# Kernel optimization log

Hardware: AMD Instinct MI355X
Metric: run time of the kernel (lower is better)

Reference implementation:

```python
import jax, jax.numpy as jnp
import numpy as np


def setup_inputs() -> dict:
    key = jax.random.key(0)
    kA, kB = jax.random.split(key)
    A = jax.random.normal(kA, (8, 256, 256, 64), dtype=jnp.float32)
    B = jax.random.normal(kB, (8, 256, 256, 64), dtype=jnp.float32)
    return {"A": A, "B": B}


def reference(A, B):
    # t-product: FFT along tube dim, batched complex matmul per frequency, IFFT.
    Af = jnp.fft.fft(A, axis=-1)          # [b, n1, n2, n3] complex
    Bf = jnp.fft.fft(B, axis=-1)          # [b, n2, n,  n3] complex
    # single batched complex GEMM over (b, n3) instead of a python loop
    Cf = jnp.einsum('bijk,bjnk->bink', Af, Bf)  # [b, n1, n, n3]
    C = jnp.fft.ifft(Cf, axis=-1)
    return jnp.real(C)
```

## Files before the change

### kernel.cpp

```cpp
#include <hip/hip_runtime.h>
#include <hip/hip_bf16.h>
#include <stdint.h>


typedef __bf16 bf16x8 __attribute__((ext_vector_type(8)));
typedef float f32x4 __attribute__((ext_vector_type(4)));

constexpr float TWC[32] = {
  1.0f, 0.99518472667f, 0.98078528040f, 0.95694033573f,
  0.92387953251f, 0.88192126435f, 0.83146961230f, 0.77301045336f,
  0.70710678119f, 0.63439328416f, 0.55557023302f, 0.47139673683f,
  0.38268343236f, 0.29028467725f, 0.19509032202f, 0.09801714033f,
  0.0f, -0.09801714033f, -0.19509032202f, -0.29028467725f,
  -0.38268343236f, -0.47139673683f, -0.55557023302f, -0.63439328416f,
  -0.70710678119f, -0.77301045336f, -0.83146961230f, -0.88192126435f,
  -0.92387953251f, -0.95694033573f, -0.98078528040f, -0.99518472667f
};
constexpr float TWS[32] = {
  0.0f, 0.09801714033f, 0.19509032202f, 0.29028467725f,
  0.38268343236f, 0.47139673683f, 0.55557023302f, 0.63439328416f,
  0.70710678119f, 0.77301045336f, 0.83146961230f, 0.88192126435f,
  0.92387953251f, 0.95694033573f, 0.98078528040f, 0.99518472667f,
  1.0f, 0.99518472667f, 0.98078528040f, 0.95694033573f,
  0.92387953251f, 0.88192126435f, 0.83146961230f, 0.77301045336f,
  0.70710678119f, 0.63439328416f, 0.55557023302f, 0.47139673683f,
  0.38268343236f, 0.29028467725f, 0.19509032202f, 0.09801714033f
};

__device__ __forceinline__ constexpr int rev6(int x) {
  int r = 0;
  for (int b = 0; b < 6; ++b) r = (r << 1) | ((x >> b) & 1);
  return r;
}

template <int SIGN>
__device__ __forceinline__ void fft64(float* re, float* im) {
#pragma unroll
  for (int i = 0; i < 64; ++i) {
    const int j = rev6(i);
    if (j > i) {
      float tr = re[i]; re[i] = re[j]; re[j] = tr;
      float ti = im[i]; im[i] = im[j]; im[j] = ti;
    }
  }
#pragma unroll
  for (int s = 0; s < 6; ++s) {
    const int half = 1 << s;
    const int m = 2 << s;
    const int tstep = 64 >> (s + 1);
#pragma unroll
    for (int kb = 0; kb < 64; kb += m) {
#pragma unroll
      for (int t = 0; t < half; ++t) {
        const int idx = t * tstep;
        const float wr = TWC[idx];
        const float wi = SIGN * TWS[idx];
        const int a = kb + t, b = a + half;
        const float xr = re[b] * wr - im[b] * wi;
        const float xi = re[b] * wi + im[b] * wr;
        re[b] = re[a] - xr; im[b] = im[a] - xi;
        re[a] += xr;        im[a] += xi;
      }
    }
  }
}

__global__ __launch_bounds__(64) void fft_a_kernel(const float* __restrict__ A,
                                                   __bf16* __restrict__ Af) {
  const int blk = blockIdx.x;
  const int jblk = blk & 3;
  const int bi = blk >> 2;
  const int l = threadIdx.x;
  const int lm16 = l & 15, lq4 = l >> 4;
  __shared__ float lds[64 * 68];
  const float* src = A + (((size_t)bi * 256) + (size_t)jblk * 64) * 64;
#pragma unroll
  for (int it = 0; it < 16; ++it) {
    const int r = it * 4 + lq4;
    const float4 v = *(const float4*)&src[(size_t)r * 64 + lm16 * 4];
    *(float4*)&lds[r * 68 + lm16 * 4] = v;
  }
  __syncthreads();
  float re[64], im[64];
#pragma unroll
  for (int e = 0; e < 64; ++e) { re[e] = lds[l * 68 + e]; im[e] = 0.0f; }
  fft64<-1>(re, im);
  const int b = bi >> 8, i = bi & 255;
  const int j = jblk * 64 + l;
#pragma unroll
  for (int k = 0; k <= 32; ++k) {
    const size_t plane = (size_t)(b * 33 + k) * (256 * 512);
    Af[plane + (size_t)i * 512 + j]       = (__bf16)re[k];
    Af[plane + (size_t)i * 512 + 256 + j] = (__bf16)im[k];
  }
}

__global__ __launch_bounds__(64) void fft_b_kernel(const float* __restrict__ B,
                                                   __bf16* __restrict__ Bn) {
  const int blk = blockIdx.x;
  const int jblk = blk & 3;
  const int bn = blk >> 2;
  const int b = bn >> 8, n = bn & 255;
  const int l = threadIdx.x;
  const int lm16 = l & 15, lq4 = l >> 4;
  __shared__ float lds[64 * 68];
#pragma unroll
  for (int it = 0; it < 16; ++it) {
    const int r = it * 4 + lq4;
    const size_t base = (((size_t)b * 256 + (size_t)(jblk * 64 + r)) * 256 + n) * 64;
    const float4 v = *(const float4*)&B[base + lm16 * 4];
    *(float4*)&lds[r * 68 + lm16 * 4] = v;
  }
  __syncthreads();
  float re[64], im[64];
#pragma unroll
  for (int e = 0; e < 64; ++e) { re[e] = lds[l * 68 + e]; im[e] = 0.0f; }
  fft64<-1>(re, im);
  const int j = jblk * 64 + l;
#pragma unroll
  for (int k = 0; k <= 32; ++k) {
    const size_t plane = (size_t)(b * 33 + k) * (256 * 512);
    Bn[plane + (size_t)n * 512 + j]       = (__bf16)re[k];
    Bn[plane + (size_t)n * 512 + 256 + j] = (__bf16)im[k];
  }
}

__device__ __forceinline__ void gload_lds16(const void* g, void* l) {
  __builtin_amdgcn_global_load_lds(
      (const __attribute__((address_space(1))) void*)g,
      (__attribute__((address_space(3))) void*)l, 16, 0, 0);
}

__device__ __forceinline__ bf16x8 neg8(bf16x8 v) {
  union { bf16x8 b; uint32_t u[4]; } x;
  x.b = v;
  x.u[0] ^= 0x80008000u; x.u[1] ^= 0x80008000u;
  x.u[2] ^= 0x80008000u; x.u[3] ^= 0x80008000u;
  return x.b;
}

__global__ __launch_bounds__(256, 2) void gemm_kernel(const __bf16* __restrict__ Af,
                                                      const __bf16* __restrict__ Bn,
                                                      __bf16* __restrict__ Cf) {
  const int bid = blockIdx.x;
  const int x = bid & 7, qx = bid >> 3;
  const int g = x * 33 + (qx >> 2);
  const int tile = qx & 3;
  const int i0 = (tile >> 1) * 128, n0 = (tile & 1) * 128;

  const int tid = threadIdx.x;
  const int lane = tid & 63, wv = tid >> 6;
  const int wm = wv >> 1, wn = wv & 1;
  const int lm = lane & 15, qq = lane >> 4;

  __shared__ __bf16 S[4][128 * 32];

  const __bf16* aPlane = Af + (size_t)g * (256 * 512);
  const __bf16* bPlane = Bn + (size_t)g * (256 * 512);

  const int row_in = lane >> 2;
  const int c_phys = lane & 3;
  const int c_log = c_phys ^ ((row_in >> 1) & 3);
  const __bf16* stageBase = (wv < 2 ? aPlane : bPlane);
  const int r0 = (wv < 2 ? i0 : n0);
  const int colOff = (wv & 1) * 256;
  const __bf16* gsrc0 = stageBase + (size_t)(r0 + row_in) * 512 + colOff + c_log * 8;
  char* ldst = (char*)&S[wv][0];

  f32x4 acc_r[4][4], acc_i[4][4];
#pragma unroll
  for (int mi = 0; mi < 4; ++mi)
#pragma unroll
    for (int ni = 0; ni < 4; ++ni) {
      acc_r[mi][ni] = f32x4{0.f, 0.f, 0.f, 0.f};
      acc_i[mi][ni] = f32x4{0.f, 0.f, 0.f, 0.f};
    }

  int aoff[4], boff[4];
#pragma unroll
  for (int mi = 0; mi < 4; ++mi) {
    const int R = wm * 64 + mi * 16 + lm;
    aoff[mi] = R * 32 + ((qq ^ ((R >> 1) & 3)) * 8);
  }
#pragma unroll
  for (int ni = 0; ni < 4; ++ni) {
    const int R = wn * 64 + ni * 16 + lm;
    boff[ni] = R * 32 + ((qq ^ ((R >> 1) & 3)) * 8);
  }

  for (int kt = 0; kt < 8; ++kt) {
#pragma unroll
    for (int p = 0; p < 8; ++p) {
      gload_lds16(gsrc0 + (size_t)p * 16 * 512 + kt * 32, ldst + p * 1024);
    }
    __syncthreads();

    bf16x8 ar[4], ai[4], br[4], bi[4], nbi[4];
#pragma unroll
    for (int mi = 0; mi < 4; ++mi) {
      ar[mi] = *(const bf16x8*)&S[0][aoff[mi]];
      ai[mi] = *(const bf16x8*)&S[1][aoff[mi]];
    }
#pragma unroll
    for (int ni = 0; ni < 4; ++ni) {
      br[ni]  = *(const bf16x8*)&S[2][boff[ni]];
      bi[ni]  = *(const bf16x8*)&S[3][boff[ni]];
      nbi[ni] = neg8(bi[ni]);
    }
#pragma unroll
    for (int mi = 0; mi < 4; ++mi)
#pragma unroll
      for (int ni = 0; ni < 4; ++ni) {
        acc_r[mi][ni] = __builtin_amdgcn_mfma_f32_16x16x32_bf16(ar[mi], br[ni],  acc_r[mi][ni], 0, 0, 0);
        acc_r[mi][ni] = __builtin_amdgcn_mfma_f32_16x16x32_bf16(ai[mi], nbi[ni], acc_r[mi][ni], 0, 0, 0);
        acc_i[mi][ni] = __builtin_amdgcn_mfma_f32_16x16x32_bf16(ar[mi], bi[ni],  acc_i[mi][ni], 0, 0, 0);
        acc_i[mi][ni] = __builtin_amdgcn_mfma_f32_16x16x32_bf16(ai[mi], br[ni],  acc_i[mi][ni], 0, 0, 0);
      }
    __syncthreads();
  }

  __bf16* cPlane = Cf + (size_t)g * (256 * 512);
#pragma unroll
  for (int mi = 0; mi < 4; ++mi)
#pragma unroll
    for (int ni = 0; ni < 4; ++ni) {
      const int col = n0 + wn * 64 + ni * 16 + lm;
#pragma unroll
      for (int r = 0; r < 4; ++r) {
        const int row = i0 + wm * 64 + mi * 16 + qq * 4 + r;
        cPlane[(size_t)row * 512 + col]       = (__bf16)acc_r[mi][ni][r];
        cPlane[(size_t)row * 512 + 256 + col] = (__bf16)acc_i[mi][ni][r];
      }
    }
}

__global__ __launch_bounds__(64) void ifft_kernel(const __bf16* __restrict__ Cf,
                                                  float* __restrict__ C) {
  const int blk = blockIdx.x;
  const int nblk = blk & 3;
  const int bi = blk >> 2;
  const int b = bi >> 8, i = bi & 255;
  const int l = threadIdx.x;
  const int lm16 = l & 15, lq4 = l >> 4;
  const int n = nblk * 64 + l;
  float re[64], im[64];
#pragma unroll
  for (int k = 0; k <= 32; ++k) {
    const size_t plane = (size_t)(b * 33 + k) * (256 * 512);
    const float cr = (float)Cf[plane + (size_t)i * 512 + n];
    const float ci = (float)Cf[plane + (size_t)i * 512 + 256 + n];
    re[k] = cr; im[k] = ci;
    if (k >= 1 && k <= 31) { re[64 - k] = cr; im[64 - k] = -ci; }
  }
  fft64<1>(re, im);
  __shared__ float lds[64 * 68];
#pragma unroll
  for (int t = 0; t < 64; ++t) lds[l * 68 + t] = re[t] * (1.0f / 64.0f);
  __syncthreads();
  const size_t base = (((size_t)b * 256 + i) * 256 + (size_t)nblk * 64) * 64;
#pragma unroll
  for (int it = 0; it < 16; ++it) {
    const int r = it * 4 + lq4;
    const float4 v = *(const float4*)&lds[r * 68 + lm16 * 4];
    *(float4*)&C[base + (size_t)r * 64 + lm16 * 4] = v;
  }
}

extern "C" void kernel_launch(void* const* d_in, const int* in_sizes, int n_in,
                              void* d_out, int out_size, void* d_ws, size_t ws_size,
                              hipStream_t stream) {
  const float* A = (const float*)d_in[0];
  const float* B = (const float*)d_in[1];
  float* C = (float*)d_out;

  char* ws = (char*)d_ws;
  const size_t planeBytes = (size_t)264 * 256 * 512 * 2;
  __bf16* Af = (__bf16*)ws;
  __bf16* Bn = (__bf16*)(ws + planeBytes);
  __bf16* Cf = (__bf16*)(ws + 2 * planeBytes);

  fft_a_kernel<<<8192, 64, 0, stream>>>(A, Af);
  fft_b_kernel<<<8192, 64, 0, stream>>>(B, Bn);
  gemm_kernel<<<1056, 256, 0, stream>>>(Af, Bn, Cf);
  ifft_kernel<<<8192, 64, 0, stream>>>(Cf, C);
}
```

Baseline: 419.1 us.

## Merge forward FFT kernels and vectorize bf16 spectral stores/loads via LDS staging

Merges the A and B forward FFT kernels into a single launch. Each kernel now stages its bf16 spectra through LDS so it writes 16-byte coalesced chunks instead of scattered 2-byte stores. The inverse FFT kernel now loads its bf16 input with global_load_lds 16-byte transfers into LDS instead of per-element 2-byte global loads. The aim is to cut memory transaction overhead and one launch, at the cost of extra LDS round trips and barriers.

```diff
diff --git a/kernel.cpp b/kernel.cpp
--- a/kernel.cpp
+++ b/kernel.cpp
@@ -65,70 +65,81 @@
   }
 }
 
-__global__ __launch_bounds__(64) void fft_a_kernel(const float* __restrict__ A,
-                                                   __bf16* __restrict__ Af) {
-  const int blk = blockIdx.x;
-  const int jblk = blk & 3;
-  const int bi = blk >> 2;
-  const int l = threadIdx.x;
-  const int lm16 = l & 15, lq4 = l >> 4;
-  __shared__ float lds[64 * 68];
-  const float* src = A + (((size_t)bi * 256) + (size_t)jblk * 64) * 64;
-#pragma unroll
-  for (int it = 0; it < 16; ++it) {
-    const int r = it * 4 + lq4;
-    const float4 v = *(const float4*)&src[(size_t)r * 64 + lm16 * 4];
-    *(float4*)&lds[r * 68 + lm16 * 4] = v;
-  }
-  __syncthreads();
-  float re[64], im[64];
-#pragma unroll
-  for (int e = 0; e < 64; ++e) { re[e] = lds[l * 68 + e]; im[e] = 0.0f; }
-  fft64<-1>(re, im);
-  const int b = bi >> 8, i = bi & 255;
-  const int j = jblk * 64 + l;
-#pragma unroll
-  for (int k = 0; k <= 32; ++k) {
-    const size_t plane = (size_t)(b * 33 + k) * (256 * 512);
-    Af[plane + (size_t)i * 512 + j]       = (__bf16)re[k];
-    Af[plane + (size_t)i * 512 + 256 + j] = (__bf16)im[k];
-  }
-}
-
-__global__ __launch_bounds__(64) void fft_b_kernel(const float* __restrict__ B,
-                                                   __bf16* __restrict__ Bn) {
-  const int blk = blockIdx.x;
-  const int jblk = blk & 3;
-  const int bn = blk >> 2;
-  const int b = bn >> 8, n = bn & 255;
-  const int l = threadIdx.x;
-  const int lm16 = l & 15, lq4 = l >> 4;
-  __shared__ float lds[64 * 68];
-#pragma unroll
-  for (int it = 0; it < 16; ++it) {
-    const int r = it * 4 + lq4;
-    const size_t base = (((size_t)b * 256 + (size_t)(jblk * 64 + r)) * 256 + n) * 64;
-    const float4 v = *(const float4*)&B[base + lm16 * 4];
-    *(float4*)&lds[r * 68 + lm16 * 4] = v;
-  }
-  __syncthreads();
-  float re[64], im[64];
-#pragma unroll
-  for (int e = 0; e < 64; ++e) { re[e] = lds[l * 68 + e]; im[e] = 0.0f; }
-  fft64<-1>(re, im);
-  const int j = jblk * 64 + l;
-#pragma unroll
-  for (int k = 0; k <= 32; ++k) {
-    const size_t plane = (size_t)(b * 33 + k) * (256 * 512);
-    Bn[plane + (size_t)n * 512 + j]       = (__bf16)re[k];
-    Bn[plane + (size_t)n * 512 + 256 + j] = (__bf16)im[k];
-  }
-}
-
 __device__ __forceinline__ void gload_lds16(const void* g, void* l) {
   __builtin_amdgcn_global_load_lds(
       (const __attribute__((address_space(1))) void*)g,
       (__attribute__((address_space(3))) void*)l, 16, 0, 0);
+}
+
+__global__ __launch_bounds__(64) void fft_ab_kernel(const float* __restrict__ A,
+                                                    const float* __restrict__ B,
+                                                    __bf16* __restrict__ Af,
+                                                    __bf16* __restrict__ Bn) {
+  const int blk0 = blockIdx.x;
+  const bool isA = blk0 < 8192;
+  const int blk = blk0 & 8191;
+  const int jblk = blk & 3;
+  const int bi = blk >> 2;
+  const int b = bi >> 8, rc = bi & 255;
+  const int l = threadIdx.x;
+  const int lm16 = l & 15, lq4 = l >> 4;
+
+  __shared__ float lds[64 * 68];
+
+  const float* srcBase = isA
+      ? (A + ((size_t)bi * 256 + (size_t)jblk * 64) * 64)
+      : (B + (((size_t)b * 256 + (size_t)jblk * 64) * 256 + rc) * 64);
+  const size_t strideR = isA ? 64 : (size_t)256 * 64;
+  __bf16* dst = isA ? Af : Bn;
+
+#pragma unroll
+  for (int it = 0; it < 16; ++it) {
+    const int r = it * 4 + lq4;
+    const float4 v = *(const float4*)&srcBase[(size_t)r * strideR + lm16 * 4];
+    *(float4*)&lds[r * 68 + lm16 * 4] = v;
+  }
+  __syncthreads();
+  float re[64], im[64];
+#pragma unroll
+  for (int e = 0; e < 64; ++e) { re[e] = lds[l * 68 + e]; im[e] = 0.0f; }
+  __syncthreads();
+  fft64<-1>(re, im);
+
+  uint32_t* out32 = (uint32_t*)lds;
+#pragma unroll
+  for (int k = 0; k <= 32; ++k) {
+    union { __bf16 h[2]; uint32_t u; } pk;
+    pk.h[0] = (__bf16)re[k]; pk.h[1] = (__bf16)im[k];
+    out32[k * 68 + l] = pk.u;
+  }
+  __syncthreads();
+
+  const int hiIm = (l >> 3) & 1;
+  const int j0c = (l & 7) * 8;
+#pragma unroll
+  for (int it = 0; it < 9; ++it) {
+    const int k = it * 4 + lq4;
+    if (it < 8 || l < 16) {
+      const uint4 q0 = *(const uint4*)&out32[k * 68 + j0c];
+      const uint4 q1 = *(const uint4*)&out32[k * 68 + j0c + 4];
+      uint32_t d0, d1, d2, d3;
+      if (!hiIm) {
+        d0 = (q0.x & 0xffffu) | (q0.y << 16);
+        d1 = (q0.z & 0xffffu) | (q0.w << 16);
+        d2 = (q1.x & 0xffffu) | (q1.y << 16);
+        d3 = (q1.z & 0xffffu) | (q1.w << 16);
+      } else {
+        d0 = (q0.x >> 16) | (q0.y & 0xffff0000u);
+        d1 = (q0.z >> 16) | (q0.w & 0xffff0000u);
+        d2 = (q1.x >> 16) | (q1.y & 0xffff0000u);
+        d3 = (q1.z >> 16) | (q1.w & 0xffff0000u);
+      }
+      const size_t elem = (size_t)(b * 33 + k) * (256 * 512)
+                        + (size_t)rc * 512 + hiIm * 256 + jblk * 64 + (l & 7) * 8;
+      uint4 outv; outv.x = d0; outv.y = d1; outv.z = d2; outv.w = d3;
+      *(uint4*)&dst[elem] = outv;
+    }
+  }
 }
 
 __device__ __forceinline__ bf16x8 neg8(bf16x8 v) {
@@ -242,18 +253,33 @@
   const int b = bi >> 8, i = bi & 255;
   const int l = threadIdx.x;
   const int lm16 = l & 15, lq4 = l >> 4;
-  const int n = nblk * 64 + l;
+
+  __shared__ float lds[64 * 68];
+  __bf16* in16 = (__bf16*)lds;
+
+  const int hiIm = (l >> 3) & 1;
+  const int j0c = (l & 7) * 8;
+  const size_t gbase = (size_t)i * 512 + (size_t)hiIm * 256 + (size_t)nblk * 64 + j0c;
+#pragma unroll
+  for (int it = 0; it < 9; ++it) {
+    const int k = it * 4 + lq4;
+    if (it < 8 || l < 16) {
+      const __bf16* g = Cf + (size_t)(b * 33 + k) * (256 * 512) + gbase;
+      gload_lds16(g, (char*)in16 + it * 1024);
+    }
+  }
+  __syncthreads();
+
   float re[64], im[64];
 #pragma unroll
   for (int k = 0; k <= 32; ++k) {
-    const size_t plane = (size_t)(b * 33 + k) * (256 * 512);
-    const float cr = (float)Cf[plane + (size_t)i * 512 + n];
-    const float ci = (float)Cf[plane + (size_t)i * 512 + 256 + n];
+    const float cr = (float)in16[k * 128 + l];
+    const float ci = (float)in16[k * 128 + 64 + l];
     re[k] = cr; im[k] = ci;
     if (k >= 1 && k <= 31) { re[64 - k] = cr; im[64 - k] = -ci; }
   }
+  __syncthreads();
   fft64<1>(re, im);
-  __shared__ float lds[64 * 68];
 #pragma unroll
   for (int t = 0; t < 64; ++t) lds[l * 68 + t] = re[t] * (1.0f / 64.0f);
   __syncthreads();
@@ -279,8 +305,7 @@
   __bf16* Bn = (__bf16*)(ws + planeBytes);
   __bf16* Cf = (__bf16*)(ws + 2 * planeBytes);
 
-  fft_a_kernel<<<8192, 64, 0, stream>>>(A, Af);
-  fft_b_kernel<<<8192, 64, 0, stream>>>(B, Bn);
+  fft_ab_kernel<<<16384, 64, 0, stream>>>(A, B, Af, Bn);
   gemm_kernel<<<1056, 256, 0, stream>>>(Af, Bn, Cf);
   ifft_kernel<<<8192, 64, 0, stream>>>(Cf, C);
 }
```

Measured after the change: 415.7 us. Within noise of the previous version (-0.8%).
